# Kernel tuning notes

Hardware: AMD Instinct MI355X
Metric: run time of the kernel (lower is better)

## Reference

```python
import jax, jax.numpy as jnp
import numpy as np

B, T, I, H, O = 32, 128, 256, 256, 128

def setup_inputs() -> dict:
    key = jax.random.key(0)
    k = jax.random.split(key, 7)
    init_k = 1.0 / np.sqrt(H)
    sentence = jax.random.normal(k[0], (B, T, I), dtype=jnp.float32)
    weight_lambda = jax.random.uniform(k[1], (H, H + I), minval=0.0, maxval=1.0, dtype=jnp.float32)
    weight_gamma = jax.random.uniform(k[2], (H, H + I), minval=-0.001 * init_k, maxval=0.001 * init_k, dtype=jnp.float32)
    weight = jax.random.uniform(k[3], (H, H + I), minval=-init_k, maxval=init_k, dtype=jnp.float32)
    bias = jax.random.uniform(k[4], (H,), minval=-init_k, maxval=init_k, dtype=jnp.float32)
    W_out = jax.random.uniform(k[5], (O, H), minval=-init_k, maxval=init_k, dtype=jnp.float32)
    b_out = jax.random.uniform(k[6], (O,), minval=-init_k, maxval=init_k, dtype=jnp.float32)
    return {"sentence": sentence, "weight_lambda": weight_lambda, "weight_gamma": weight_gamma,
            "weight": weight, "bias": bias, "W_out": W_out, "b_out": b_out}

def reference(sentence, weight_lambda, weight_gamma, weight, bias, W_out, b_out):
    b = sentence.shape[0]
    h0 = jnp.zeros((b, H), dtype=sentence.dtype)
    F0 = jnp.zeros((b, H, H + I), dtype=sentence.dtype)

    def step(carry, x_t):
        h, F = carry
        total_input = jnp.concatenate([x_t, h], axis=1)           # (B, I+H)
        total_weights = weight + F                                 # (B, H, I+H)
        h_new = jnp.tanh(jnp.einsum('bf,bhf->bh', total_input, total_weights) + bias)
        norm = jnp.linalg.norm(total_weights, axis=2, keepdims=True) + 1e-16  # (B, H, 1)
        h_new = h_new / norm[..., 0]
        F_new = weight_lambda * (F / norm) + weight_gamma * jnp.einsum('bf,bh->bhf', total_input, h_new)
        return (h_new, F_new), None

    (h_T, F_T), _ = jax.lax.scan(step, (h0, F0), jnp.swapaxes(sentence, 0, 1))
    tag_space = h_T @ W_out.T + b_out
    return tag_space, h_T, F_T
```

## Files before the change

kernel.cpp:

```cpp
#include <hip/hip_runtime.h>

#define BB 32
#define TT 128
#define II 256
#define HH 256
#define OO 128
#define FWID 512


typedef unsigned long long u64;
typedef float f32x2 __attribute__((ext_vector_type(2)));

__device__ __forceinline__ f32x2 mk2(float a, float b) { f32x2 r; r.x = a; r.y = b; return r; }

__device__ __forceinline__ f32x2 pk_fma(f32x2 a, f32x2 b, f32x2 c) {
    f32x2 d;
    asm("v_pk_fma_f32 %0, %1, %2, %3" : "=v"(d) : "v"(a), "v"(b), "v"(c));
    return d;
}
__device__ __forceinline__ f32x2 pk_mul(f32x2 a, f32x2 b) {
    f32x2 d;
    asm("v_pk_mul_f32 %0, %1, %2" : "=v"(d) : "v"(a), "v"(b));
    return d;
}
__device__ __forceinline__ f32x2 pk_add(f32x2 a, f32x2 b) {
    f32x2 d;
    asm("v_pk_add_f32 %0, %1, %2" : "=v"(d) : "v"(a), "v"(b));
    return d;
}

template<int CTRL>
__device__ __forceinline__ float dpp_add(float x) {
    int t = __builtin_amdgcn_update_dpp(0, __float_as_int(x), CTRL, 0xF, 0xF, true);
    return x + __int_as_float(t);
}
__device__ __forceinline__ float row16_sum(float x) {
    x = dpp_add<0x128>(x);
    x = dpp_add<0x124>(x);
    x = dpp_add<0x122>(x);
    x = dpp_add<0x121>(x);
    return x;
}
__device__ __forceinline__ void row16_sum2(float& a, float& b) {
    a = dpp_add<0x128>(a); b = dpp_add<0x128>(b);
    a = dpp_add<0x124>(a); b = dpp_add<0x124>(b);
    a = dpp_add<0x122>(a); b = dpp_add<0x122>(b);
    a = dpp_add<0x121>(a); b = dpp_add<0x121>(b);
}

__device__ __forceinline__ u64 slot_ld(const u64* p) {
    return __hip_atomic_load(p, __ATOMIC_RELAXED, __HIP_MEMORY_SCOPE_AGENT);
}

__device__ __forceinline__ void gather_to_lds(const u64* base, int lane, unsigned us,
                                              float* dst, int* flag, int fval) {
    const u64* p = base + 4 * lane;
    u64 a, b, c, d;
    {
        u64 a0 = slot_ld(p), b0 = slot_ld(p + 1), c0 = slot_ld(p + 2), d0 = slot_ld(p + 3);
        for (;;) {
            u64 a1 = slot_ld(p), b1 = slot_ld(p + 1), c1 = slot_ld(p + 2), d1 = slot_ld(p + 3);
            bool ok0 = ((unsigned)(a0 >> 32) >= us) & ((unsigned)(b0 >> 32) >= us) &
                       ((unsigned)(c0 >> 32) >= us) & ((unsigned)(d0 >> 32) >= us);
            if (__all(ok0)) { a = a0; b = b0; c = c0; d = d0; break; }
            a0 = slot_ld(p); b0 = slot_ld(p + 1); c0 = slot_ld(p + 2); d0 = slot_ld(p + 3);
            bool ok1 = ((unsigned)(a1 >> 32) >= us) & ((unsigned)(b1 >> 32) >= us) &
                       ((unsigned)(c1 >> 32) >= us) & ((unsigned)(d1 >> 32) >= us);
            if (__all(ok1)) { a = a1; b = b1; c = c1; d = d1; break; }
        }
    }
    float4 hv;
    hv.x = __uint_as_float((unsigned)a);
    hv.y = __uint_as_float((unsigned)b);
    hv.z = __uint_as_float((unsigned)c);
    hv.w = __uint_as_float((unsigned)d);
    *reinterpret_cast<float4*>(dst + 4 * lane) = hv;
    if (lane == 0)
        __hip_atomic_store(flag, fval, __ATOMIC_RELEASE, __HIP_MEMORY_SCOPE_WORKGROUP);
}

__global__ __launch_bounds__(512, 2)
void stpn_kernel(const float* __restrict__ x,
                 const float* __restrict__ wlam,
                 const float* __restrict__ wgam,
                 const float* __restrict__ w,
                 const float* __restrict__ bias,
                 const float* __restrict__ wout,
                 const float* __restrict__ bout,
                 float* __restrict__ out,
                 u64* __restrict__ slots)
{
    __shared__ __align__(16) float lh[2][HH];
    __shared__ int lflag[2];

    const int tid  = threadIdx.x;
    const int bk   = blockIdx.x;
    const int b    = bk & 31;
    const int sl   = bk >> 5;
    const int wv   = tid >> 6;
    const int lane = tid & 63;
    const int g    = tid >> 4;
    const int i    = tid & 15;
    const int r    = sl * 32 + (g & 31);

    if (tid < 2) lflag[tid] = 0;

    f32x2 W2[16], Lm2[16], G2[16], F2[16];
    {
        const float4* wr = reinterpret_cast<const float4*>(w    + (size_t)r * FWID);
        const float4* lr = reinterpret_cast<const float4*>(wlam + (size_t)r * FWID);
        const float4* gr = reinterpret_cast<const float4*>(wgam + (size_t)r * FWID);
#pragma unroll
        for (int k = 0; k < 8; ++k) {
            float4 t;
            t = wr[k * 16 + i]; W2[2*k]  = mk2(t.x, t.y); W2[2*k+1]  = mk2(t.z, t.w);
            t = lr[k * 16 + i]; Lm2[2*k] = mk2(t.x, t.y); Lm2[2*k+1] = mk2(t.z, t.w);
            t = gr[k * 16 + i]; G2[2*k]  = mk2(t.x, t.y); G2[2*k+1]  = mk2(t.z, t.w);
            F2[2*k] = mk2(0.f, 0.f); F2[2*k+1] = mk2(0.f, 0.f);
        }
    }
    const float bj = bias[r];
    float hl = 0.f;

    float4 px0, px1, px2, px3;
    {
        const float4* xb4 = reinterpret_cast<const float4*>(x + (size_t)b * TT * II);
        px0 = xb4[i]; px1 = xb4[16 + i]; px2 = xb4[32 + i]; px3 = xb4[48 + i];
    }

    __syncthreads();

    for (int s = 0; s < TT; ++s) {
        const int par = s & 1;

        f32x2 X2[8];
        X2[0] = mk2(px0.x, px0.y); X2[1] = mk2(px0.z, px0.w);
        X2[2] = mk2(px1.x, px1.y); X2[3] = mk2(px1.z, px1.w);
        X2[4] = mk2(px2.x, px2.y); X2[5] = mk2(px2.z, px2.w);
        X2[6] = mk2(px3.x, px3.y); X2[7] = mk2(px3.z, px3.w);

        f32x2 tw2[8];
        f32x2 dx2 = mk2(0.f, 0.f), nv2 = mk2(0.f, 0.f);
#pragma unroll
        for (int j = 0; j < 8; ++j) {
            f32x2 t = pk_add(W2[j], F2[j]);
            dx2 = pk_fma(X2[j], t, dx2);
            nv2 = pk_fma(t, t, nv2);
        }
#pragma unroll
        for (int j = 0; j < 8; ++j) {
            tw2[j] = pk_add(W2[8 + j], F2[8 + j]);
            nv2 = pk_fma(tw2[j], tw2[j], nv2);
        }
        float dxs = dx2.x + dx2.y;
        float nrm = nv2.x + nv2.y;
        row16_sum2(dxs, nrm);
        const float invn = __builtin_amdgcn_rsqf(nrm);
        const f32x2 invn2 = mk2(invn, invn);
        const float dxb = dxs + bj;

#pragma unroll
        for (int j = 0; j < 16; ++j) F2[j] = pk_mul(Lm2[j], pk_mul(F2[j], invn2));

        if (wv == 0) {
            __builtin_amdgcn_s_setprio(1);
            gather_to_lds(slots + ((size_t)par * BB + b) * HH, lane,
                          (unsigned)s, lh[par], &lflag[par], s + 1);
            __builtin_amdgcn_s_setprio(0);
        }

        while (__hip_atomic_load(&lflag[par], __ATOMIC_ACQUIRE, __HIP_MEMORY_SCOPE_WORKGROUP) <= s) {
            __builtin_amdgcn_s_sleep(1);
        }
        const float4* lh4 = reinterpret_cast<const float4*>(lh[par]);
        float4 ha = lh4[i], hb = lh4[16 + i], hc = lh4[32 + i], hd = lh4[48 + i];
        f32x2 H2[8];
        H2[0] = mk2(ha.x, ha.y); H2[1] = mk2(ha.z, ha.w);
        H2[2] = mk2(hb.x, hb.y); H2[3] = mk2(hb.z, hb.w);
        H2[4] = mk2(hc.x, hc.y); H2[5] = mk2(hc.z, hc.w);
        H2[6] = mk2(hd.x, hd.y); H2[7] = mk2(hd.z, hd.w);

        f32x2 a2 = pk_mul(H2[0], tw2[0]);
        f32x2 b2 = pk_mul(H2[1], tw2[1]);
        a2 = pk_fma(H2[2], tw2[2], a2);
        b2 = pk_fma(H2[3], tw2[3], b2);
        a2 = pk_fma(H2[4], tw2[4], a2);
        b2 = pk_fma(H2[5], tw2[5], b2);
        a2 = pk_fma(H2[6], tw2[6], a2);
        b2 = pk_fma(H2[7], tw2[7], b2);
        f32x2 c2 = pk_add(a2, b2);
        float dh = c2.x + c2.y;
        dh = row16_sum(dh);

        const float e = __expf(2.0f * (dxb + dh));
        const float h = (1.0f - 2.0f * __builtin_amdgcn_rcpf(e + 1.0f)) * invn;
        hl = h;

        if (i == 0) {
            __hip_atomic_store(slots + ((size_t)(par ^ 1) * BB + b) * HH + r,
                               ((u64)(unsigned)(s + 1) << 32) | (unsigned)__float_as_uint(h),
                               __ATOMIC_RELAXED, __HIP_MEMORY_SCOPE_AGENT);
        }

        if (s + 1 < TT) {
            const float4* xn = reinterpret_cast<const float4*>(x + ((size_t)b * TT + (s + 1)) * II);
            px0 = xn[i]; px1 = xn[16 + i]; px2 = xn[32 + i]; px3 = xn[48 + i];
        }

        const f32x2 h2v = mk2(h, h);
#pragma unroll
        for (int j = 0; j < 8; ++j)
            F2[j] = pk_fma(pk_mul(X2[j], G2[j]), h2v, F2[j]);
#pragma unroll
        for (int j = 0; j < 8; ++j)
            F2[8 + j] = pk_fma(pk_mul(G2[8 + j], H2[j]), h2v, F2[8 + j]);
    }

    {
        float4* fo = reinterpret_cast<float4*>(out + 12288 + ((size_t)b * HH + r) * FWID);
#pragma unroll
        for (int k = 0; k < 8; ++k) {
            float4 v;
            v.x = F2[2*k].x; v.y = F2[2*k].y; v.z = F2[2*k+1].x; v.w = F2[2*k+1].y;
            fo[k * 16 + i] = v;
        }
    }
    if (i == 0) out[4096 + (size_t)b * HH + r] = hl;

    if (sl == 0) {
        if (wv == 0) {
            gather_to_lds(slots + ((size_t)(TT & 1) * BB + b) * HH, lane,
                          (unsigned)TT, lh[0], &lflag[0], TT + 1);
        }
        while (__hip_atomic_load(&lflag[0], __ATOMIC_ACQUIRE, __HIP_MEMORY_SCOPE_WORKGROUP) <= TT) {
            __builtin_amdgcn_s_sleep(1);
        }
        if (tid < OO) {
            const float* hv = lh[0];
            float acc = bout[tid];
            const float* wo = wout + (size_t)tid * HH;
#pragma unroll 4
            for (int jj = 0; jj < HH; ++jj) acc = fmaf(wo[jj], hv[jj], acc);
            out[(size_t)b * OO + tid] = acc;
        }
    }
}

extern "C" void kernel_launch(void* const* d_in, const int* in_sizes, int n_in,
                              void* d_out, int out_size, void* d_ws, size_t ws_size,
                              hipStream_t stream) {
    (void)in_sizes; (void)n_in; (void)out_size; (void)ws_size;
    const float* x    = (const float*)d_in[0];
    const float* wlam = (const float*)d_in[1];
    const float* wgam = (const float*)d_in[2];
    const float* w    = (const float*)d_in[3];
    const float* bias = (const float*)d_in[4];
    const float* wout = (const float*)d_in[5];
    const float* bout = (const float*)d_in[6];
    float* out = (float*)d_out;

    u64* slots = (u64*)d_ws;

    hipMemsetAsync(d_ws, 0, 2ull * BB * HH * 8ull, stream);

    hipLaunchKernelGGL(stpn_kernel, dim3(256), dim3(512), 0, stream,
                       x, wlam, wgam, w, bias, wout, bout, out, slots);
}
```

Baseline: 242.8 us.

## Replace per-launch slot memset with epoch-tagged global slots and simplified polling

Removes the hipMemsetAsync that cleared the exchange slots before each launch. It instead keeps a persistent device-global slot array and tags each hidden value with an epoch base taken from a global run counter, so stale values from earlier launches are never read as current. Step 0 skips the gather because h0 is zero. The double-buffered polling loop is replaced by inline-asm loads and a store with sc0 sc1 cache bits. This saves a separate memset launch and one wait per run, but depends on every launch using exactly 256 blocks to keep the counter arithmetic consistent, and uses hand-written cache-control asm.

```diff
diff --git a/kernel.cpp b/kernel.cpp
--- a/kernel.cpp
+++ b/kernel.cpp
@@ -11,6 +11,9 @@
 typedef unsigned long long u64;
 typedef float f32x2 __attribute__((ext_vector_type(2)));
 
+__device__ u64 g_slots[2ull * BB * HH];
+__device__ unsigned g_run_ctr = 0;
+
 __device__ __forceinline__ f32x2 mk2(float a, float b) { f32x2 r; r.x = a; r.y = b; return r; }
 
 __device__ __forceinline__ f32x2 pk_fma(f32x2 a, f32x2 b, f32x2 c) {
@@ -48,26 +51,23 @@
     a = dpp_add<0x121>(a); b = dpp_add<0x121>(b);
 }
 
-__device__ __forceinline__ u64 slot_ld(const u64* p) {
-    return __hip_atomic_load(p, __ATOMIC_RELAXED, __HIP_MEMORY_SCOPE_AGENT);
-}
-
-__device__ __forceinline__ void gather_to_lds(const u64* base, int lane, unsigned us,
+__device__ __forceinline__ void gather_to_lds(const u64* base_p, int lane, unsigned us,
                                               float* dst, int* flag, int fval) {
-    const u64* p = base + 4 * lane;
+    const u64* p = base_p + 4 * lane;
     u64 a, b, c, d;
-    {
-        u64 a0 = slot_ld(p), b0 = slot_ld(p + 1), c0 = slot_ld(p + 2), d0 = slot_ld(p + 3);
-        for (;;) {
-            u64 a1 = slot_ld(p), b1 = slot_ld(p + 1), c1 = slot_ld(p + 2), d1 = slot_ld(p + 3);
-            bool ok0 = ((unsigned)(a0 >> 32) >= us) & ((unsigned)(b0 >> 32) >= us) &
-                       ((unsigned)(c0 >> 32) >= us) & ((unsigned)(d0 >> 32) >= us);
-            if (__all(ok0)) { a = a0; b = b0; c = c0; d = d0; break; }
-            a0 = slot_ld(p); b0 = slot_ld(p + 1); c0 = slot_ld(p + 2); d0 = slot_ld(p + 3);
-            bool ok1 = ((unsigned)(a1 >> 32) >= us) & ((unsigned)(b1 >> 32) >= us) &
-                       ((unsigned)(c1 >> 32) >= us) & ((unsigned)(d1 >> 32) >= us);
-            if (__all(ok1)) { a = a1; b = b1; c = c1; d = d1; break; }
-        }
+    for (;;) {
+        asm volatile(
+            "global_load_dwordx2 %0, %4, off sc0 sc1\n\t"
+            "global_load_dwordx2 %1, %4, off offset:8 sc0 sc1\n\t"
+            "global_load_dwordx2 %2, %4, off offset:16 sc0 sc1\n\t"
+            "global_load_dwordx2 %3, %4, off offset:24 sc0 sc1\n\t"
+            "s_waitcnt vmcnt(0)"
+            : "=&v"(a), "=&v"(b), "=&v"(c), "=&v"(d)
+            : "v"(p)
+            : "memory");
+        bool ok = ((unsigned)(a >> 32) >= us) & ((unsigned)(b >> 32) >= us) &
+                  ((unsigned)(c >> 32) >= us) & ((unsigned)(d >> 32) >= us);
+        if (__all(ok)) break;
     }
     float4 hv;
     hv.x = __uint_as_float((unsigned)a);
@@ -87,11 +87,11 @@
                  const float* __restrict__ bias,
                  const float* __restrict__ wout,
                  const float* __restrict__ bout,
-                 float* __restrict__ out,
-                 u64* __restrict__ slots)
+                 float* __restrict__ out)
 {
     __shared__ __align__(16) float lh[2][HH];
     __shared__ int lflag[2];
+    __shared__ unsigned sbase;
 
     const int tid  = threadIdx.x;
     const int bk   = blockIdx.x;
@@ -103,6 +103,11 @@
     const int i    = tid & 15;
     const int r    = sl * 32 + (g & 31);
 
+    if (tid == 0) {
+        unsigned my = __hip_atomic_fetch_add(&g_run_ctr, 1u,
+                          __ATOMIC_RELAXED, __HIP_MEMORY_SCOPE_AGENT);
+        sbase = (my >> 8) * 130u;
+    }
     if (tid < 2) lflag[tid] = 0;
 
     f32x2 W2[16], Lm2[16], G2[16], F2[16];
@@ -129,6 +134,7 @@
     }
 
     __syncthreads();
+    const unsigned base = sbase;
 
     for (int s = 0; s < TT; ++s) {
         const int par = s & 1;
@@ -162,18 +168,22 @@
 #pragma unroll
         for (int j = 0; j < 16; ++j) F2[j] = pk_mul(Lm2[j], pk_mul(F2[j], invn2));
 
-        if (wv == 0) {
-            __builtin_amdgcn_s_setprio(1);
-            gather_to_lds(slots + ((size_t)par * BB + b) * HH, lane,
-                          (unsigned)s, lh[par], &lflag[par], s + 1);
-            __builtin_amdgcn_s_setprio(0);
-        }
-
-        while (__hip_atomic_load(&lflag[par], __ATOMIC_ACQUIRE, __HIP_MEMORY_SCOPE_WORKGROUP) <= s) {
-            __builtin_amdgcn_s_sleep(1);
-        }
-        const float4* lh4 = reinterpret_cast<const float4*>(lh[par]);
-        float4 ha = lh4[i], hb = lh4[16 + i], hc = lh4[32 + i], hd = lh4[48 + i];
+        float4 ha, hb, hc, hd;
+        if (s != 0) {
+            if (wv == 0) {
+                __builtin_amdgcn_s_setprio(1);
+                gather_to_lds(g_slots + ((size_t)par * BB + b) * HH, lane,
+                              base + (unsigned)s, lh[par], &lflag[par], s + 1);
+                __builtin_amdgcn_s_setprio(0);
+            }
+            while (__hip_atomic_load(&lflag[par], __ATOMIC_ACQUIRE, __HIP_MEMORY_SCOPE_WORKGROUP) <= s) {
+                __builtin_amdgcn_s_sleep(1);
+            }
+            const float4* lh4 = reinterpret_cast<const float4*>(lh[par]);
+            ha = lh4[i]; hb = lh4[16 + i]; hc = lh4[32 + i]; hd = lh4[48 + i];
+        } else {
+            ha = make_float4(0.f, 0.f, 0.f, 0.f); hb = ha; hc = ha; hd = ha;
+        }
         f32x2 H2[8];
         H2[0] = mk2(ha.x, ha.y); H2[1] = mk2(ha.z, ha.w);
         H2[2] = mk2(hb.x, hb.y); H2[3] = mk2(hb.z, hb.w);
@@ -197,9 +207,9 @@
         hl = h;
 
         if (i == 0) {
-            __hip_atomic_store(slots + ((size_t)(par ^ 1) * BB + b) * HH + r,
-                               ((u64)(unsigned)(s + 1) << 32) | (unsigned)__float_as_uint(h),
-                               __ATOMIC_RELAXED, __HIP_MEMORY_SCOPE_AGENT);
+            const u64 val = ((u64)(base + (unsigned)s + 1u) << 32) | (unsigned)__float_as_uint(h);
+            u64* ptr = g_slots + ((size_t)(par ^ 1) * BB + b) * HH + r;
+            asm volatile("global_store_dwordx2 %0, %1, off sc0 sc1" :: "v"(ptr), "v"(val) : "memory");
         }
 
         if (s + 1 < TT) {
@@ -229,8 +239,8 @@
 
     if (sl == 0) {
         if (wv == 0) {
-            gather_to_lds(slots + ((size_t)(TT & 1) * BB + b) * HH, lane,
-                          (unsigned)TT, lh[0], &lflag[0], TT + 1);
+            gather_to_lds(g_slots + ((size_t)(TT & 1) * BB + b) * HH, lane,
+                          base + (unsigned)TT, lh[0], &lflag[0], TT + 1);
         }
         while (__hip_atomic_load(&lflag[0], __ATOMIC_ACQUIRE, __HIP_MEMORY_SCOPE_WORKGROUP) <= TT) {
             __builtin_amdgcn_s_sleep(1);
@@ -249,7 +259,7 @@
 extern "C" void kernel_launch(void* const* d_in, const int* in_sizes, int n_in,
                               void* d_out, int out_size, void* d_ws, size_t ws_size,
                               hipStream_t stream) {
-    (void)in_sizes; (void)n_in; (void)out_size; (void)ws_size;
+    (void)in_sizes; (void)n_in; (void)out_size; (void)d_ws; (void)ws_size;
     const float* x    = (const float*)d_in[0];
     const float* wlam = (const float*)d_in[1];
     const float* wgam = (const float*)d_in[2];
@@ -259,10 +269,6 @@
     const float* bout = (const float*)d_in[6];
     float* out = (float*)d_out;
 
-    u64* slots = (u64*)d_ws;
-
-    hipMemsetAsync(d_ws, 0, 2ull * BB * HH * 8ull, stream);
-
     hipLaunchKernelGGL(stpn_kernel, dim3(256), dim3(512), 0, stream,
-                       x, wlam, wgam, w, bias, wout, bout, out, slots);
-}
+                       x, wlam, wgam, w, bias, wout, bout, out);
+}
```

Result: no change. 247.1 us (+1.8%).
